# Kernel optimization log

Measured on AMD Instinct MI355X. Metric: run time of the kernel, lower is better.

The kernel has to match this reference:

```python
import jax, jax.numpy as jnp
import numpy as np

DEMBED = 512
DMODEL = 512
HEAD = 8
B, L = 4, 2048


def setup_inputs() -> dict:
    key = jax.random.key(0)
    ks = jax.random.split(key, 12)
    s_in = 1.0 / np.sqrt(DEMBED)
    s_out = 1.0 / np.sqrt(DMODEL)
    return {
        "x_q": jax.random.normal(ks[0], (B, L, DEMBED), jnp.float32),
        "x_k": jax.random.normal(ks[1], (B, L, DEMBED), jnp.float32),
        "x_v": jax.random.normal(ks[2], (B, L, DEMBED), jnp.float32),
        "mask": jax.random.randint(ks[3], (B, L, L), 0, 2, jnp.int32),
        "Wq": jax.random.uniform(ks[4], (DMODEL, DEMBED), jnp.float32, -s_in, s_in),
        "bq": jnp.zeros((DMODEL,), jnp.float32),
        "Wk": jax.random.uniform(ks[5], (DMODEL, DEMBED), jnp.float32, -s_in, s_in),
        "bk": jnp.zeros((DMODEL,), jnp.float32),
        "Wv": jax.random.uniform(ks[6], (DMODEL, DEMBED), jnp.float32, -s_in, s_in),
        "bv": jnp.zeros((DMODEL,), jnp.float32),
        "Wo": jax.random.uniform(ks[7], (DEMBED, DMODEL), jnp.float32, -s_out, s_out),
        "bo": jnp.zeros((DEMBED,), jnp.float32),
    }


def _split_heads(x):
    # [B, L, D] -> [B, head, L, h_dv]; head h gets contiguous channels h*h_dv:(h+1)*h_dv,
    # matching torch's transpose(1,2).reshape(B,head,h_dv,L).transpose(2,3)
    b, l, d = x.shape
    return x.reshape(b, l, HEAD, d // HEAD).transpose(0, 2, 1, 3)


def reference(x_q, x_k, x_v, mask, Wq, bq, Wk, bk, Wv, bv, Wo, bo):
    q = _split_heads(x_q @ Wq.T + bq)  # [B, H, L, hd]
    k = _split_heads(x_k @ Wk.T + bk)
    v = _split_heads(x_v @ Wv.T + bv)
    h_dv = q.shape[-1]
    scores = jnp.einsum("bhqd,bhkd->bhqk", q, k) / np.sqrt(h_dv)
    scores = scores + mask[:, None, :, :].astype(scores.dtype) * (-1e30)
    attn = jax.nn.softmax(scores, axis=-1)
    out = jnp.einsum("bhqk,bhkd->bhqd", attn, v)  # [B, H, L, hd]
    out = out.transpose(0, 2, 1, 3).reshape(x_q.shape[0], x_q.shape[1], DMODEL)
    final = out @ Wo.T + bo
    return final, attn
```

## Files before the change

kernel.cpp:

```cpp
#include <hip/hip_runtime.h>

typedef unsigned short u16;
typedef __attribute__((ext_vector_type(8))) short short8;
typedef __attribute__((ext_vector_type(4))) float f32x4;

#define DE 512
#define SL 2048
#define NB 4
#define NH 8
#define HD 64

__device__ __forceinline__ float bf2f(u16 h) {
    union { unsigned u; float f; } v; v.u = ((unsigned)h) << 16; return v.f;
}
__device__ __forceinline__ u16 f2bf(float f) {
    union { float f; unsigned u; } v; v.f = f;
    unsigned u = v.u;
    return (u16)((u + 0x7FFFu + ((u >> 16) & 1u)) >> 16);
}
__device__ __forceinline__ short8 ld8f(const float* __restrict__ p) {
    const float4 a = *(const float4*)p;
    const float4 b = *(const float4*)(p + 4);
    short8 r;
    ((u16*)&r)[0] = f2bf(a.x); ((u16*)&r)[1] = f2bf(a.y);
    ((u16*)&r)[2] = f2bf(a.z); ((u16*)&r)[3] = f2bf(a.w);
    ((u16*)&r)[4] = f2bf(b.x); ((u16*)&r)[5] = f2bf(b.y);
    ((u16*)&r)[6] = f2bf(b.z); ((u16*)&r)[7] = f2bf(b.w);
    return r;
}

__global__ __launch_bounds__(256) void cvt3(const float* __restrict__ s0,
                                            const float* __restrict__ s1,
                                            const float* __restrict__ s2,
                                            u16* __restrict__ dst, int per) {
    const float* src = (blockIdx.y == 0) ? s0 : ((blockIdx.y == 1) ? s1 : s2);
    const int idx = (blockIdx.x * 256 + threadIdx.x) * 8;
    if (idx >= per) return;
    short8 v = ld8f(src + idx);
    *(short8*)(dst + (size_t)blockIdx.y * per + idx) = v;
}

__device__ __forceinline__ void llds16(const u16* g, u16* l) {
    __builtin_amdgcn_global_load_lds((const __attribute__((address_space(1))) void*)g,
                                     (__attribute__((address_space(3))) void*)l, 16, 0, 0);
}

__device__ __forceinline__ void gemm64_body(u16* As, u16* Bs,
                                            const u16* __restrict__ X,
                                            const u16* __restrict__ W,
                                            const float* __restrict__ bias,
                                            void* __restrict__ outv,
                                            int mode, int tok0, int col0) {
    const int tid = threadIdx.x;
    const int l = tid & 63, w = tid >> 6;
    const int q16 = l & 15, quad = l >> 4;
    const int wr = w >> 1, wc = w & 1;

    const int srow = tid >> 3;
    const int scol = ((tid & 7) ^ (srow & 7)) * 8;
    const u16* ga = X + (size_t)(tok0 + srow) * DE + scol;
    const u16* gb = W + (size_t)(col0 + srow) * DE + scol;
    u16* la = As + tid * 8;
    u16* lb = Bs + tid * 8;

    f32x4 acc[2][2] = {};

    #pragma unroll
    for (int i = 0; i < 2; ++i) {
        llds16(ga + (size_t)i * 32 * DE, la + i * 2048);
        llds16(gb + (size_t)i * 32 * DE, lb + i * 2048);
    }
    __syncthreads();

    int cur = 0;
    for (int ks = 64; ks <= DE; ks += 64) {
        if (ks < DE) {
            u16* da = la + (cur ^ 1) * 4096;
            u16* db = lb + (cur ^ 1) * 4096;
            #pragma unroll
            for (int i = 0; i < 2; ++i) {
                llds16(ga + (size_t)i * 32 * DE + ks, da + i * 2048);
                llds16(gb + (size_t)i * 32 * DE + ks, db + i * 2048);
            }
        }
        const char* Ab = (const char*)(As + cur * 4096);
        const char* Bb = (const char*)(Bs + cur * 4096);
        #pragma unroll
        for (int kk = 0; kk < 64; kk += 32) {
            short8 af[2], bf[2];
            #pragma unroll
            for (int m = 0; m < 2; ++m) {
                const int row = wr * 32 + m * 16 + q16;
                af[m] = *(const short8*)(Ab + row * 128 + (((kk + quad * 8) * 2) ^ ((q16 & 7) << 4)));
            }
            #pragma unroll
            for (int n = 0; n < 2; ++n) {
                const int row = wc * 32 + n * 16 + q16;
                bf[n] = *(const short8*)(Bb + row * 128 + (((kk + quad * 8) * 2) ^ ((q16 & 7) << 4)));
            }
            #pragma unroll
            for (int m = 0; m < 2; ++m)
                #pragma unroll
                for (int n = 0; n < 2; ++n)
                    acc[m][n] = __builtin_amdgcn_mfma_f32_16x16x32_bf16(af[m], bf[n], acc[m][n], 0, 0, 0);
        }
        __syncthreads();
        cur ^= 1;
    }

    #pragma unroll
    for (int n = 0; n < 2; ++n) {
        const int col = col0 + wc * 32 + n * 16 + q16;
        const float bv = bias[col];
        #pragma unroll
        for (int m = 0; m < 2; ++m) {
            const f32x4 a4 = acc[m][n];
            const int tg0 = tok0 + wr * 32 + m * 16 + quad * 4;
            if (mode == 2) {
                const int b = tg0 >> 11, t0 = tg0 & 2047;
                const int h = col >> 6, d = col & 63;
                ushort4 pk;
                pk.x = f2bf(a4[0] + bv); pk.y = f2bf(a4[1] + bv);
                pk.z = f2bf(a4[2] + bv); pk.w = f2bf(a4[3] + bv);
                *(ushort4*)((u16*)outv + ((size_t)((b * NH + h) * HD + d) << 11) + t0) = pk;
            } else if (mode == 1) {
                const int h = col >> 6, d = col & 63;
                #pragma unroll
                for (int r = 0; r < 4; ++r) {
                    const int tg = tg0 + r;
                    const int b = tg >> 11, t = tg & 2047;
                    ((u16*)outv)[(((size_t)(b * NH + h) * SL + t) << 6) + d] = f2bf(a4[r] + bv);
                }
            } else {
                #pragma unroll
                for (int r = 0; r < 4; ++r)
                    ((float*)outv)[(size_t)(tg0 + r) * DE + col] = a4[r] + bv;
            }
        }
    }
}

__global__ __launch_bounds__(256) void gemm_qkv(const u16* __restrict__ xbf,
                                                const u16* __restrict__ wbf,
                                                const float* __restrict__ bq,
                                                const float* __restrict__ bk,
                                                const float* __restrict__ bv,
                                                u16* __restrict__ outbase) {
    __shared__ __align__(16) u16 As[2][4096];
    __shared__ __align__(16) u16 Bs[2][4096];
    const int z = blockIdx.z;
    const u16* X = xbf + (size_t)z * 4194304;
    const u16* W = wbf + (size_t)z * 262144;
    const float* bias = (z == 0) ? bq : ((z == 1) ? bk : bv);
    u16* out = outbase + (size_t)z * 4194304;
    gemm64_body(&As[0][0], &Bs[0][0], X, W, bias, out,
                (z == 2) ? 2 : 1, blockIdx.x * 64, blockIdx.y * 64);
}

__global__ __launch_bounds__(256) void gemm_fin(const u16* __restrict__ X,
                                                const u16* __restrict__ W,
                                                const float* __restrict__ bias,
                                                float* __restrict__ outp) {
    __shared__ __align__(16) u16 As[2][4096];
    __shared__ __align__(16) u16 Bs[2][4096];
    gemm64_body(&As[0][0], &Bs[0][0], X, W, bias, outp,
                0, blockIdx.x * 64, blockIdx.y * 64);
}

__global__ __launch_bounds__(512) void attn_kernel(const u16* __restrict__ Q,
                                                   const u16* __restrict__ K,
                                                   const u16* __restrict__ Vt,
                                                   const int* __restrict__ mask,
                                                   float* __restrict__ attn_out,
                                                   u16* __restrict__ Obuf) {
    __shared__ __align__(16) u16 P[16][2056];
    __shared__ float partial[16][8];
    __shared__ float linv[16];
    __shared__ float ored[4][16][16];

    const int tid = threadIdx.x;
    const int lane = tid & 63, wave = tid >> 6;
    const int q16 = lane & 15, quad = lane >> 4;
    const int qblk = blockIdx.x, h = blockIdx.y, b = blockIdx.z;
    const int qbase = qblk * 16;

    const u16* qplane = Q + (size_t)((b * NH + h) * SL) * HD;
    const u16* kplane = K + (size_t)((b * NH + h) * SL) * HD;

    const u16* qrow = qplane + (qbase + q16) * HD + quad * 8;
    const short8 aq0 = *(const short8*)(qrow);
    const short8 aq1 = *(const short8*)(qrow + 32);

    const int qg0 = qbase + quad * 4;
    const int* mbase = mask + (size_t)(b * SL + qg0) * SL;
    const int k0 = wave * 256;
    float rs0 = 0.f, rs1 = 0.f, rs2 = 0.f, rs3 = 0.f;
    #pragma unroll 2
    for (int kt = 0; kt < 16; ++kt) {
        const int kbase = k0 + kt * 16;
        const u16* krow = kplane + (kbase + q16) * HD + quad * 8;
        short8 b0 = *(const short8*)(krow);
        short8 b1 = *(const short8*)(krow + 32);
        f32x4 s = {};
        s = __builtin_amdgcn_mfma_f32_16x16x32_bf16(aq0, b0, s, 0, 0, 0);
        s = __builtin_amdgcn_mfma_f32_16x16x32_bf16(aq1, b1, s, 0, 0, 0);
        const int* mrow = mbase + kbase + q16;
        const float u0 = mrow[0]          ? 0.0f : __expf(s[0] * 0.125f);
        const float u1 = mrow[SL]         ? 0.0f : __expf(s[1] * 0.125f);
        const float u2 = mrow[2 * SL]     ? 0.0f : __expf(s[2] * 0.125f);
        const float u3 = mrow[3 * SL]     ? 0.0f : __expf(s[3] * 0.125f);
        rs0 += u0; rs1 += u1; rs2 += u2; rs3 += u3;
        P[quad * 4 + 0][kbase + q16] = f2bf(u0);
        P[quad * 4 + 1][kbase + q16] = f2bf(u1);
        P[quad * 4 + 2][kbase + q16] = f2bf(u2);
        P[quad * 4 + 3][kbase + q16] = f2bf(u3);
    }
    #pragma unroll
    for (int off = 1; off < 16; off <<= 1) {
        rs0 += __shfl_xor(rs0, off);
        rs1 += __shfl_xor(rs1, off);
        rs2 += __shfl_xor(rs2, off);
        rs3 += __shfl_xor(rs3, off);
    }
    if (q16 == 0) {
        partial[quad * 4 + 0][wave] = rs0;
        partial[quad * 4 + 1][wave] = rs1;
        partial[quad * 4 + 2][wave] = rs2;
        partial[quad * 4 + 3][wave] = rs3;
    }
    __syncthreads();

    if (tid < 16) {
        float s = 0.f;
        #pragma unroll
        for (int w = 0; w < 8; ++w) s += partial[tid][w];
        linv[tid] = 1.0f / s;
    }
    __syncthreads();

    {
        const int r3 = tid >> 5, cseg = tid & 31;
        const float inv = linv[r3];
        const size_t rowbase = ((size_t)((b * NH + h) * SL + qbase + r3)) * SL;
        #pragma unroll
        for (int i = 0; i < 8; ++i) {
            const int c = cseg * 8 + i * 256;
            short8 v = *(const short8*)&P[r3][c];
            f32x4 w0, w1;
            w0[0] = bf2f(((u16*)&v)[0]) * inv;
            w0[1] = bf2f(((u16*)&v)[1]) * inv;
            w0[2] = bf2f(((u16*)&v)[2]) * inv;
            w0[3] = bf2f(((u16*)&v)[3]) * inv;
            w1[0] = bf2f(((u16*)&v)[4]) * inv;
            w1[1] = bf2f(((u16*)&v)[5]) * inv;
            w1[2] = bf2f(((u16*)&v)[6]) * inv;
            w1[3] = bf2f(((u16*)&v)[7]) * inv;
            __builtin_nontemporal_store(w0, (f32x4*)(attn_out + rowbase + c));
            __builtin_nontemporal_store(w1, (f32x4*)(attn_out + rowbase + c + 4));
        }
    }

    const int dt = wave & 3, kh = wave >> 2;
    const u16* vplane = Vt + (size_t)((b * NH + h) * HD) * SL;
    f32x4 o = {};
    const int kstart = kh * 1024;
    #pragma unroll 4
    for (int kk = kstart; kk < kstart + 1024; kk += 32) {
        short8 a = *(const short8*)&P[q16][kk + quad * 8];
        short8 bv = *(const short8*)(vplane + (dt * 16 + q16) * SL + kk + quad * 8);
        o = __builtin_amdgcn_mfma_f32_16x16x32_bf16(a, bv, o, 0, 0, 0);
    }
    if (kh == 1) {
        #pragma unroll
        for (int rr = 0; rr < 4; ++rr) ored[dt][quad * 4 + rr][q16] = o[rr];
    }
    __syncthreads();
    if (kh == 0) {
        #pragma unroll
        for (int rr = 0; rr < 4; ++rr) {
            const int row = quad * 4 + rr;
            const float val = (o[rr] + ored[dt][row][q16]) * linv[row];
            const int qg = qbase + row;
            Obuf[(size_t)(b * SL + qg) * DE + h * HD + dt * 16 + q16] = f2bf(val);
        }
    }
}

extern "C" void kernel_launch(void* const* d_in, const int* in_sizes, int n_in,
                              void* d_out, int out_size, void* d_ws, size_t ws_size,
                              hipStream_t stream) {
    const float* x_q = (const float*)d_in[0];
    const float* x_k = (const float*)d_in[1];
    const float* x_v = (const float*)d_in[2];
    const int* mask = (const int*)d_in[3];
    const float* Wq = (const float*)d_in[4];
    const float* bq = (const float*)d_in[5];
    const float* Wk = (const float*)d_in[6];
    const float* bk = (const float*)d_in[7];
    const float* Wv = (const float*)d_in[8];
    const float* bv = (const float*)d_in[9];
    const float* Wo = (const float*)d_in[10];
    const float* bo = (const float*)d_in[11];

    u16* ws = (u16*)d_ws;
    u16* qb = ws;
    u16* vt = ws + 2 * 4194304;
    u16* ob = ws + 3 * 4194304;

    float* outp = (float*)d_out;
    float* attn_out = outp + 4194304;

    u16* xbf = (u16*)attn_out;
    u16* wbf = xbf + 3 * 4194304;

    cvt3<<<dim3(2048, 3), 256, 0, stream>>>(x_q, x_k, x_v, xbf, 4194304);
    cvt3<<<dim3(128, 3), 256, 0, stream>>>(Wq, Wk, Wv, wbf, 262144);

    gemm_qkv<<<dim3(128, 8, 3), 256, 0, stream>>>(xbf, wbf, bq, bk, bv, ws);

    attn_kernel<<<dim3(128, 8, 4), 512, 0, stream>>>(qb, ws + 4194304, vt, mask, attn_out, ob);

    cvt3<<<dim3(128, 1), 256, 0, stream>>>(Wo, Wo, Wo, qb, 262144);
    gemm_fin<<<dim3(128, 8), 256, 0, stream>>>(ob, qb, bo, outp);
}
```

Measured before the change: 880.1 us.

## Transpose QK^T MFMA operands for coalesced mask loads and prefetch K tiles

Swaps the A/B operands of the score MFMA so each lane holds four consecutive key columns of one query row. The mask can then be read as a single int4 per lane instead of four strided scalar loads, and P is written as a packed 8-byte store. The row-sum reduction shrinks to two shuffles. It also software-prefetches the next K tile and mask vector one iteration ahead, adds s_setprio around the MFMA sections, and sets a min-blocks launch bound, which may push up register pressure.

```diff
diff --git a/kernel.cpp b/kernel.cpp
--- a/kernel.cpp
+++ b/kernel.cpp
@@ -167,12 +167,12 @@
                 0, blockIdx.x * 64, blockIdx.y * 64);
 }
 
-__global__ __launch_bounds__(512) void attn_kernel(const u16* __restrict__ Q,
-                                                   const u16* __restrict__ K,
-                                                   const u16* __restrict__ Vt,
-                                                   const int* __restrict__ mask,
-                                                   float* __restrict__ attn_out,
-                                                   u16* __restrict__ Obuf) {
+__global__ __launch_bounds__(512, 4) void attn_kernel(const u16* __restrict__ Q,
+                                                      const u16* __restrict__ K,
+                                                      const u16* __restrict__ Vt,
+                                                      const int* __restrict__ mask,
+                                                      float* __restrict__ attn_out,
+                                                      u16* __restrict__ Obuf) {
     __shared__ __align__(16) u16 P[16][2056];
     __shared__ float partial[16][8];
     __shared__ float linv[16];
@@ -191,43 +191,45 @@
     const short8 aq0 = *(const short8*)(qrow);
     const short8 aq1 = *(const short8*)(qrow + 32);
 
-    const int qg0 = qbase + quad * 4;
-    const int* mbase = mask + (size_t)(b * SL + qg0) * SL;
     const int k0 = wave * 256;
-    float rs0 = 0.f, rs1 = 0.f, rs2 = 0.f, rs3 = 0.f;
+    const int* mrowp = mask + (size_t)(b * SL + qbase + q16) * SL;
+    float rs = 0.f;
+
+    const u16* krow = kplane + (k0 + q16) * HD + quad * 8;
+    short8 b0 = *(const short8*)(krow);
+    short8 b1 = *(const short8*)(krow + 32);
+    int4 m4 = *(const int4*)(mrowp + k0 + quad * 4);
+
     #pragma unroll 2
     for (int kt = 0; kt < 16; ++kt) {
-        const int kbase = k0 + kt * 16;
-        const u16* krow = kplane + (kbase + q16) * HD + quad * 8;
-        short8 b0 = *(const short8*)(krow);
-        short8 b1 = *(const short8*)(krow + 32);
+        const int kb = k0 + kt * 16;
+        const int knext = kb + ((kt < 15) ? 16 : 0);
+        const u16* krow2 = kplane + (knext + q16) * HD + quad * 8;
+        short8 nb0 = *(const short8*)(krow2);
+        short8 nb1 = *(const short8*)(krow2 + 32);
+        int4 nm4 = *(const int4*)(mrowp + knext + quad * 4);
+
         f32x4 s = {};
-        s = __builtin_amdgcn_mfma_f32_16x16x32_bf16(aq0, b0, s, 0, 0, 0);
-        s = __builtin_amdgcn_mfma_f32_16x16x32_bf16(aq1, b1, s, 0, 0, 0);
-        const int* mrow = mbase + kbase + q16;
-        const float u0 = mrow[0]          ? 0.0f : __expf(s[0] * 0.125f);
-        const float u1 = mrow[SL]         ? 0.0f : __expf(s[1] * 0.125f);
-        const float u2 = mrow[2 * SL]     ? 0.0f : __expf(s[2] * 0.125f);
-        const float u3 = mrow[3 * SL]     ? 0.0f : __expf(s[3] * 0.125f);
-        rs0 += u0; rs1 += u1; rs2 += u2; rs3 += u3;
-        P[quad * 4 + 0][kbase + q16] = f2bf(u0);
-        P[quad * 4 + 1][kbase + q16] = f2bf(u1);
-        P[quad * 4 + 2][kbase + q16] = f2bf(u2);
-        P[quad * 4 + 3][kbase + q16] = f2bf(u3);
-    }
-    #pragma unroll
-    for (int off = 1; off < 16; off <<= 1) {
-        rs0 += __shfl_xor(rs0, off);
-        rs1 += __shfl_xor(rs1, off);
-        rs2 += __shfl_xor(rs2, off);
-        rs3 += __shfl_xor(rs3, off);
-    }
-    if (q16 == 0) {
-        partial[quad * 4 + 0][wave] = rs0;
-        partial[quad * 4 + 1][wave] = rs1;
-        partial[quad * 4 + 2][wave] = rs2;
-        partial[quad * 4 + 3][wave] = rs3;
-    }
+        __builtin_amdgcn_s_setprio(1);
+        s = __builtin_amdgcn_mfma_f32_16x16x32_bf16(b0, aq0, s, 0, 0, 0);
+        s = __builtin_amdgcn_mfma_f32_16x16x32_bf16(b1, aq1, s, 0, 0, 0);
+        __builtin_amdgcn_s_setprio(0);
+
+        const float u0 = m4.x ? 0.0f : __expf(s[0] * 0.125f);
+        const float u1 = m4.y ? 0.0f : __expf(s[1] * 0.125f);
+        const float u2 = m4.z ? 0.0f : __expf(s[2] * 0.125f);
+        const float u3 = m4.w ? 0.0f : __expf(s[3] * 0.125f);
+        rs += (u0 + u1) + (u2 + u3);
+        uint2 pk;
+        pk.x = (unsigned)f2bf(u0) | ((unsigned)f2bf(u1) << 16);
+        pk.y = (unsigned)f2bf(u2) | ((unsigned)f2bf(u3) << 16);
+        *(uint2*)&P[q16][kb + quad * 4] = pk;
+
+        b0 = nb0; b1 = nb1; m4 = nm4;
+    }
+    rs += __shfl_xor(rs, 16);
+    rs += __shfl_xor(rs, 32);
+    if (lane < 16) partial[lane][wave] = rs;
     __syncthreads();
 
     if (tid < 16) {
@@ -264,12 +266,14 @@
     const u16* vplane = Vt + (size_t)((b * NH + h) * HD) * SL;
     f32x4 o = {};
     const int kstart = kh * 1024;
+    __builtin_amdgcn_s_setprio(1);
     #pragma unroll 4
     for (int kk = kstart; kk < kstart + 1024; kk += 32) {
         short8 a = *(const short8*)&P[q16][kk + quad * 8];
         short8 bv = *(const short8*)(vplane + (dt * 16 + q16) * SL + kk + quad * 8);
         o = __builtin_amdgcn_mfma_f32_16x16x32_bf16(a, bv, o, 0, 0, 0);
     }
+    __builtin_amdgcn_s_setprio(0);
     if (kh == 1) {
         #pragma unroll
         for (int rr = 0; rr < 4; ++rr) ored[dt][quad * 4 + rr][q16] = o[rr];
```

Result: slower. 926.3 us (+5.3%).
